# Performance work log

Hardware: AMD Instinct MI355X
Metric: run time of the kernel (lower is better)

Reference implementation:

```python
import jax, jax.numpy as jnp
import numpy as np
import math

D_MODEL = 512
N_HEADS = 8
MAX_SEQ_LEN = 4096
DENSITY = 0.3


def _make_random_mask(key, seq_len, density=DENSITY):
    # rand < density, symmetrized via (m + m.T)/2, clamped to [0,1], diag = 1
    u = jax.random.uniform(key, (seq_len, seq_len), dtype=jnp.float32)
    m = (u < density).astype(jnp.float32)
    m = jnp.clip((m + m.T) * 0.5, 0.0, 1.0)
    return m.at[jnp.diag_indices(seq_len)].set(1.0)


def setup_inputs() -> dict:
    key = jax.random.key(0)
    ks = jax.random.split(key, 10)
    B, T, C = 2, 4096, D_MODEL
    scale = 1.0 / math.sqrt(C)
    x = jax.random.normal(ks[0], (B, T, C), dtype=jnp.float32)
    mask = _make_random_mask(ks[1], MAX_SEQ_LEN)[:T, :T]
    # Linear weights stored as (in, out): y = x @ W + b
    Wq = jax.random.normal(ks[2], (C, C), dtype=jnp.float32) * scale
    Wk = jax.random.normal(ks[3], (C, C), dtype=jnp.float32) * scale
    Wv = jax.random.normal(ks[4], (C, C), dtype=jnp.float32) * scale
    Wo = jax.random.normal(ks[5], (C, C), dtype=jnp.float32) * scale
    bq = jax.random.normal(ks[6], (C,), dtype=jnp.float32) * scale
    bk = jax.random.normal(ks[7], (C,), dtype=jnp.float32) * scale
    bv = jax.random.normal(ks[8], (C,), dtype=jnp.float32) * scale
    bo = jax.random.normal(ks[9], (C,), dtype=jnp.float32) * scale
    return {"x": x, "mask": mask, "Wq": Wq, "bq": bq, "Wk": Wk, "bk": bk,
            "Wv": Wv, "bv": bv, "Wo": Wo, "bo": bo}


def reference(x, mask, Wq, bq, Wk, bk, Wv, bv, Wo, bo):
    B, T, C = x.shape
    H = N_HEADS
    dk = C // H
    q = (x @ Wq + bq).reshape(B, T, H, dk)
    k = (x @ Wk + bk).reshape(B, T, H, dk)
    v = (x @ Wv + bv).reshape(B, T, H, dk)
    # scores: [B, H, T, T]
    attn = jnp.einsum('bthd,bshd->bhts', q, k) / math.sqrt(dk)
    attn = attn * mask[None, None, :, :]  # multiplicative mask PRE-softmax
    p = jax.nn.softmax(attn, axis=-1)
    out = jnp.einsum('bhts,bshd->bthd', p, v).reshape(B, T, C)
    return out @ Wo + bo
```

## Files before the change

### kernel.cpp

```cpp
#include <hip/hip_runtime.h>
#include <math.h>

#define D_MODEL 512
#define N_HEADS 8
#define DK 64
#define QSCALE (0.0625f * 1.44269504089f)

typedef __attribute__((ext_vector_type(8))) short short8;
typedef __attribute__((ext_vector_type(4))) float f32x4;

typedef __attribute__((address_space(1))) const unsigned as1_uint;
typedef __attribute__((address_space(3))) unsigned as3_uint;

__device__ __forceinline__ unsigned short f2bf(float f) {
    unsigned u = __builtin_bit_cast(unsigned, f);
    u = (u + 0x7fff + ((u >> 16) & 1)) >> 16;
    return (unsigned short)u;
}

__global__ __launch_bounds__(256) void cvt_x_kernel(const float* __restrict__ x,
                                                    unsigned short* __restrict__ xb, int n8)
{
    int i = blockIdx.x * 256 + threadIdx.x;
    if (i >= n8) return;
    float4 a = ((const float4*)x)[i * 2];
    float4 b = ((const float4*)x)[i * 2 + 1];
    short8 o;
    o[0] = f2bf(a.x); o[1] = f2bf(a.y); o[2] = f2bf(a.z); o[3] = f2bf(a.w);
    o[4] = f2bf(b.x); o[5] = f2bf(b.y); o[6] = f2bf(b.z); o[7] = f2bf(b.w);
    ((short8*)xb)[i] = o;
}

__global__ __launch_bounds__(256) void cvt_mask_kernel(const float* __restrict__ m,
                                                       unsigned char* __restrict__ mu, int n4)
{
    int i = blockIdx.x * 256 + threadIdx.x;
    if (i >= n4) return;
    float4 v = ((const float4*)m)[i];
    uchar4 o = { (unsigned char)(v.x * 2.0f + 0.5f),
                 (unsigned char)(v.y * 2.0f + 0.5f),
                 (unsigned char)(v.z * 2.0f + 0.5f),
                 (unsigned char)(v.w * 2.0f + 0.5f) };
    ((uchar4*)mu)[i] = o;
}

__global__ __launch_bounds__(256) void cvt_wt_kernel(const float* __restrict__ W,
                                                     unsigned short* __restrict__ Wt)
{
    __shared__ float tile[64][65];
    int t = threadIdx.x;
    int c0 = blockIdx.x * 64;
    int r0 = blockIdx.y * 64;
    #pragma unroll
    for (int i = 0; i < 16; i++) {
        int e = i * 256 + t, r = e >> 6, c = e & 63;
        tile[c][r] = W[(size_t)(r0 + r) * D_MODEL + c0 + c];
    }
    __syncthreads();
    #pragma unroll
    for (int i = 0; i < 16; i++) {
        int e = i * 256 + t, n = e >> 6, kk = e & 63;
        Wt[(size_t)(c0 + n) * D_MODEL + r0 + kk] = f2bf(tile[n][kk]);
    }
}

__global__ __launch_bounds__(512) void gemm_qkv_kernel(
    const unsigned short* __restrict__ A, const unsigned short* __restrict__ Wt,
    const float* __restrict__ bq, const float* __restrict__ bk, const float* __restrict__ bv,
    unsigned short* __restrict__ qb, unsigned short* __restrict__ kb,
    unsigned short* __restrict__ vb, int M, int T)
{
    constexpr int K = D_MODEL;
    __shared__ unsigned short As[2][128 * 32];
    __shared__ unsigned short Bs[2][128 * 32];
    int t = threadIdx.x;
    int lane = t & 63, w = t >> 6;
    int ql = lane & 15, kg = lane >> 4;
    int m0 = blockIdx.y * 128, n0 = blockIdx.x * 128;
    int wm = w >> 2, wn = w & 3;
    bool vmode = (n0 >= 1024);

    const unsigned short* srcA = A + (size_t)(m0 + (t >> 2)) * K + (t & 3) * 8;
    const unsigned short* srcB = Wt + (size_t)(n0 + (t >> 2)) * K + (t & 3) * 8;

    f32x4 acc[4][2];
    #pragma unroll
    for (int i = 0; i < 4; i++)
        #pragma unroll
        for (int j = 0; j < 2; j++) { f32x4 z = {0.f, 0.f, 0.f, 0.f}; acc[i][j] = z; }

    constexpr int NIT = K / 32;
    int cur = 0;
    __builtin_amdgcn_global_load_lds((as1_uint*)(srcA),
        (as3_uint*)((char*)&As[0][0] + w * 1024), 16, 0, 0);
    __builtin_amdgcn_global_load_lds((as1_uint*)(srcB),
        (as3_uint*)((char*)&Bs[0][0] + w * 1024), 16, 0, 0);
    __syncthreads();

    for (int it = 0; it < NIT; ++it) {
        if (it + 1 < NIT) {
            int k0 = (it + 1) * 32;
            __builtin_amdgcn_global_load_lds((as1_uint*)(srcA + k0),
                (as3_uint*)((char*)&As[cur ^ 1][0] + w * 1024), 16, 0, 0);
            __builtin_amdgcn_global_load_lds((as1_uint*)(srcB + k0),
                (as3_uint*)((char*)&Bs[cur ^ 1][0] + w * 1024), 16, 0, 0);
        }
        short8 af[4], bfr[2];
        #pragma unroll
        for (int fm = 0; fm < 4; fm++)
            af[fm] = *(const short8*)((const char*)&As[cur][0] + (wm * 64 + fm * 16 + ql) * 64 + kg * 16);
        #pragma unroll
        for (int fn = 0; fn < 2; fn++)
            bfr[fn] = *(const short8*)((const char*)&Bs[cur][0] + (wn * 32 + fn * 16 + ql) * 64 + kg * 16);
        if (vmode) {
            #pragma unroll
            for (int fm = 0; fm < 4; fm++)
                #pragma unroll
                for (int fn = 0; fn < 2; fn++)
                    acc[fm][fn] = __builtin_amdgcn_mfma_f32_16x16x32_bf16(bfr[fn], af[fm], acc[fm][fn], 0, 0, 0);
        } else {
            #pragma unroll
            for (int fm = 0; fm < 4; fm++)
                #pragma unroll
                for (int fn = 0; fn < 2; fn++)
                    acc[fm][fn] = __builtin_amdgcn_mfma_f32_16x16x32_bf16(af[fm], bfr[fn], acc[fm][fn], 0, 0, 0);
        }
        __syncthreads();
        cur ^= 1;
    }

    #pragma unroll
    for (int fm = 0; fm < 4; fm++) {
        #pragma unroll
        for (int fn = 0; fn < 2; fn++) {
            if (vmode) {
                int m = m0 + wm * 64 + fm * 16 + ql;
                int b = m / T, tt = m % T;
                #pragma unroll
                for (int r = 0; r < 4; r++) {
                    int n = (n0 - 1024) + wn * 32 + fn * 16 + kg * 4 + r;
                    float val = acc[fm][fn][r] + bv[n];
                    int h = n >> 6, d = n & 63;
                    vb[((size_t)(b * N_HEADS + h) * DK + d) * T + tt] = f2bf(val);
                }
            } else {
                int n = n0 + wn * 32 + fn * 16 + ql;
                int nn = n & 511;
                bool isq = (n0 < 512);
                float bn = isq ? bq[nn] : bk[nn];
                unsigned short* dst = isq ? qb : kb;
                int h = nn >> 6, d = nn & 63;
                #pragma unroll
                for (int r = 0; r < 4; r++) {
                    int m = m0 + wm * 64 + fm * 16 + kg * 4 + r;
                    int b = m / T, tt = m % T;
                    float val = acc[fm][fn][r] + bn;
                    if (isq) val *= QSCALE;
                    dst[((size_t)(b * N_HEADS + h) * T + tt) * DK + d] = f2bf(val);
                }
            }
        }
    }
}

__global__ __launch_bounds__(512) void gemm_out_kernel(
    const unsigned short* __restrict__ A, const unsigned short* __restrict__ Bt,
    const float* __restrict__ bias, float* __restrict__ outp, int M)
{
    constexpr int K = D_MODEL;
    __shared__ unsigned short As[2][128 * 32];
    __shared__ unsigned short Bs[2][128 * 32];
    int t = threadIdx.x;
    int lane = t & 63, w = t >> 6;
    int ql = lane & 15, kg = lane >> 4;
    int m0 = blockIdx.y * 128, n0 = blockIdx.x * 128;
    int wm = w >> 2, wn = w & 3;

    const unsigned short* srcA = A + (size_t)(m0 + (t >> 2)) * K + (t & 3) * 8;
    const unsigned short* srcB = Bt + (size_t)(n0 + (t >> 2)) * K + (t & 3) * 8;

    f32x4 acc[4][2];
    #pragma unroll
    for (int i = 0; i < 4; i++)
        #pragma unroll
        for (int j = 0; j < 2; j++) { f32x4 z = {0.f, 0.f, 0.f, 0.f}; acc[i][j] = z; }

    constexpr int NIT = K / 32;
    int cur = 0;
    __builtin_amdgcn_global_load_lds((as1_uint*)(srcA),
        (as3_uint*)((char*)&As[0][0] + w * 1024), 16, 0, 0);
    __builtin_amdgcn_global_load_lds((as1_uint*)(srcB),
        (as3_uint*)((char*)&Bs[0][0] + w * 1024), 16, 0, 0);
    __syncthreads();

    for (int it = 0; it < NIT; ++it) {
        if (it + 1 < NIT) {
            int k0 = (it + 1) * 32;
            __builtin_amdgcn_global_load_lds((as1_uint*)(srcA + k0),
                (as3_uint*)((char*)&As[cur ^ 1][0] + w * 1024), 16, 0, 0);
            __builtin_amdgcn_global_load_lds((as1_uint*)(srcB + k0),
                (as3_uint*)((char*)&Bs[cur ^ 1][0] + w * 1024), 16, 0, 0);
        }
        short8 af[4], bfr[2];
        #pragma unroll
        for (int fm = 0; fm < 4; fm++)
            af[fm] = *(const short8*)((const char*)&As[cur][0] + (wm * 64 + fm * 16 + ql) * 64 + kg * 16);
        #pragma unroll
        for (int fn = 0; fn < 2; fn++)
            bfr[fn] = *(const short8*)((const char*)&Bs[cur][0] + (wn * 32 + fn * 16 + ql) * 64 + kg * 16);
        #pragma unroll
        for (int fm = 0; fm < 4; fm++)
            #pragma unroll
            for (int fn = 0; fn < 2; fn++)
                acc[fm][fn] = __builtin_amdgcn_mfma_f32_16x16x32_bf16(af[fm], bfr[fn], acc[fm][fn], 0, 0, 0);
        __syncthreads();
        cur ^= 1;
    }

    #pragma unroll
    for (int fm = 0; fm < 4; fm++) {
        #pragma unroll
        for (int fn = 0; fn < 2; fn++) {
            int n = n0 + wn * 32 + fn * 16 + ql;
            float bn = bias[n];
            #pragma unroll
            for (int r = 0; r < 4; r++) {
                int m = m0 + wm * 64 + fm * 16 + kg * 4 + r;
                outp[(size_t)m * D_MODEL + n] = acc[fm][fn][r] + bn;
            }
        }
    }
}

__global__ __launch_bounds__(256) void attn_mfma_kernel(
    const unsigned short* __restrict__ q, const unsigned short* __restrict__ k,
    const unsigned short* __restrict__ v, const unsigned char* __restrict__ mu,
    float* __restrict__ opart, float* __restrict__ lpart, int B, int T)
{
    __shared__ unsigned short Ks[2][64 * 64];
    __shared__ unsigned short Vt[64 * 64];
    __shared__ unsigned short Ps[4][32 * 64];

    int t = threadIdx.x;
    int lane = t & 63, w = t >> 6;
    int ql = lane & 15, kg = lane >> 4;
    int bh = blockIdx.x, qt = blockIdx.y, z = blockIdx.z;
    int h = bh & (N_HEADS - 1), b = bh >> 3;
    int qr0 = qt * 128;
    int Th = T >> 1;
    int kv0 = z * Th;
    int nt = Th / 64;
    int M = B * T;

    const char* kbase = (const char*)(k + ((size_t)bh * T + kv0) * DK);
    const char* vbase = (const char*)(v + (size_t)bh * DK * T + kv0);

    int lin0 = w * 1024 + lane * 16;
    int lin1 = 4096 + lin0;
    int row0 = lin0 >> 7, row1 = lin1 >> 7;
    int sw0 = (row0 & 7) << 4, sw1 = (row1 & 7) << 4;
    const char* gK0 = kbase + (lin0 ^ sw0);
    const char* gK1 = kbase + (lin1 ^ sw1);
    const char* gV0 = vbase + (size_t)row0 * (2 * T) + ((lin0 & 127) ^ sw0);
    const char* gV1 = vbase + (size_t)row1 * (2 * T) + ((lin1 & 127) ^ sw1);

    short8 qfr[2][2];
    #pragma unroll
    for (int qf = 0; qf < 2; qf++) {
        const unsigned short* qrow = q + ((size_t)bh * T + qr0 + w * 32 + qf * 16 + ql) * DK + kg * 8;
        qfr[qf][0] = *(const short8*)(qrow);
        qfr[qf][1] = *(const short8*)(qrow + 32);
    }

    const unsigned char* mrow0 = mu + (size_t)(qr0 + w * 32 + ql) * T + kv0 + kg * 4;
    const unsigned char* mrow1 = mrow0 + (size_t)16 * T;

    f32x4 oacc[2][4];
    #pragma unroll
    for (int qf = 0; qf < 2; qf++)
        #pragma unroll
        for (int c = 0; c < 4; c++) { f32x4 zz = {0.f, 0.f, 0.f, 0.f}; oacc[qf][c] = zz; }
    float lacc0 = 0.f, lacc1 = 0.f;

    unsigned mcur0[4], mcur1[4];
    #pragma unroll
    for (int c = 0; c < 4; c++) {
        mcur0[c] = *(const unsigned*)(mrow0 + c * 16);
        mcur1[c] = *(const unsigned*)(mrow1 + c * 16);
    }
    __builtin_amdgcn_global_load_lds((as1_uint*)gK0, (as3_uint*)((char*)&Ks[0][0] + w * 1024), 16, 0, 0);
    __builtin_amdgcn_global_load_lds((as1_uint*)gK1, (as3_uint*)((char*)&Ks[0][0] + 4096 + w * 1024), 16, 0, 0);

    for (int kt = 0; kt < nt; kt++) {
        __syncthreads();
        int cur = kt & 1;
        bool havenext = (kt + 1) < nt;

        unsigned mnxt0[4], mnxt1[4];
        if (havenext) {
            const unsigned char* mp0 = mrow0 + (size_t)(kt + 1) * 64;
            const unsigned char* mp1 = mrow1 + (size_t)(kt + 1) * 64;
            #pragma unroll
            for (int c = 0; c < 4; c++) {
                mnxt0[c] = *(const unsigned*)(mp0 + c * 16);
                mnxt1[c] = *(const unsigned*)(mp1 + c * 16);
            }
            size_t ko = (size_t)(kt + 1) * 8192;
            __builtin_amdgcn_global_load_lds((as1_uint*)(gK0 + ko),
                (as3_uint*)((char*)&Ks[cur ^ 1][0] + w * 1024), 16, 0, 0);
            __builtin_amdgcn_global_load_lds((as1_uint*)(gK1 + ko),
                (as3_uint*)((char*)&Ks[cur ^ 1][0] + 4096 + w * 1024), 16, 0, 0);
        }

        if (kt > 0) {
            __builtin_amdgcn_s_setprio(1);
            #pragma unroll
            for (int ks = 0; ks < 2; ks++) {
                int pboff = (ql * 128 + ks * 64 + kg * 16) ^ ((ql & 7) << 4);
                short8 pa0 = *(const short8*)((const char*)&Ps[w][0] + pboff);
                short8 pa1 = *(const short8*)((const char*)&Ps[w][0] + 2048 + pboff);
                #pragma unroll
                for (int c2 = 0; c2 < 4; c2++) {
                    int rowd = c2 * 16 + ql;
                    short8 vb = *(const short8*)((const char*)Vt +
                                ((rowd * 128 + ks * 64 + kg * 16) ^ ((rowd & 7) << 4)));
                    oacc[0][c2] = __builtin_amdgcn_mfma_f32_16x16x32_bf16(pa0, vb, oacc[0][c2], 0, 0, 0);
                    oacc[1][c2] = __builtin_amdgcn_mfma_f32_16x16x32_bf16(pa1, vb, oacc[1][c2], 0, 0, 0);
                }
            }
            __builtin_amdgcn_s_setprio(0);
        }

        __builtin_amdgcn_sched_barrier(0);
        __builtin_amdgcn_s_barrier();
        __builtin_amdgcn_sched_barrier(0);

        {
            size_t vo = (size_t)kt * 128;
            __builtin_amdgcn_global_load_lds((as1_uint*)(gV0 + vo),
                (as3_uint*)((char*)Vt + w * 1024), 16, 0, 0);
            __builtin_amdgcn_global_load_lds((as1_uint*)(gV1 + vo),
                (as3_uint*)((char*)Vt + 4096 + w * 1024), 16, 0, 0);
        }

        f32x4 sacc[2][4];
        #pragma unroll
        for (int qf = 0; qf < 2; qf++)
            #pragma unroll
            for (int c = 0; c < 4; c++) { f32x4 zz = {0.f, 0.f, 0.f, 0.f}; sacc[qf][c] = zz; }
        __builtin_amdgcn_s_setprio(1);
        #pragma unroll
        for (int ks = 0; ks < 2; ks++) {
            #pragma unroll
            for (int c = 0; c < 4; c++) {
                int row = c * 16 + ql;
                short8 kf = *(const short8*)((const char*)&Ks[cur][0] +
                            ((row * 128 + ks * 64 + kg * 16) ^ ((row & 7) << 4)));
                sacc[0][c] = __builtin_amdgcn_mfma_f32_16x16x32_bf16(kf, qfr[0][ks], sacc[0][c], 0, 0, 0);
                sacc[1][c] = __builtin_amdgcn_mfma_f32_16x16x32_bf16(kf, qfr[1][ks], sacc[1][c], 0, 0, 0);
            }
        }
        __builtin_amdgcn_s_setprio(0);

        #pragma unroll
        for (int c = 0; c < 4; c++) {
            unsigned mw = mcur0[c];
            float p0 = __builtin_amdgcn_exp2f(sacc[0][c][0] * (float)(mw & 0xffu));
            float p1 = __builtin_amdgcn_exp2f(sacc[0][c][1] * (float)((mw >> 8) & 0xffu));
            float p2 = __builtin_amdgcn_exp2f(sacc[0][c][2] * (float)((mw >> 16) & 0xffu));
            float p3 = __builtin_amdgcn_exp2f(sacc[0][c][3] * (float)(mw >> 24));
            lacc0 += (p0 + p1) + (p2 + p3);
            unsigned lo, hi;
            asm("v_cvt_pk_bf16_f32 %0, %1, %2" : "=v"(lo) : "v"(p0), "v"(p1));
            asm("v_cvt_pk_bf16_f32 %0, %1, %2" : "=v"(hi) : "v"(p2), "v"(p3));
            int byteoff = (ql * 128 + (c * 16 + kg * 4) * 2) ^ ((ql & 7) << 4);
            uint2 pr = { lo, hi };
            *(uint2*)((char*)&Ps[w][0] + byteoff) = pr;

            unsigned nw = mcur1[c];
            float q0 = __builtin_amdgcn_exp2f(sacc[1][c][0] * (float)(nw & 0xffu));
            float q1 = __builtin_amdgcn_exp2f(sacc[1][c][1] * (float)((nw >> 8) & 0xffu));
            float q2 = __builtin_amdgcn_exp2f(sacc[1][c][2] * (float)((nw >> 16) & 0xffu));
            float q3 = __builtin_amdgcn_exp2f(sacc[1][c][3] * (float)(nw >> 24));
            lacc1 += (q0 + q1) + (q2 + q3);
            unsigned lo1, hi1;
            asm("v_cvt_pk_bf16_f32 %0, %1, %2" : "=v"(lo1) : "v"(q0), "v"(q1));
            asm("v_cvt_pk_bf16_f32 %0, %1, %2" : "=v"(hi1) : "v"(q2), "v"(q3));
            uint2 pr1 = { lo1, hi1 };
            *(uint2*)((char*)&Ps[w][0] + 2048 + byteoff) = pr1;
        }

        if (havenext) {
            #pragma unroll
            for (int c = 0; c < 4; c++) { mcur0[c] = mnxt0[c]; mcur1[c] = mnxt1[c]; }
        }
    }

    __syncthreads();
    __builtin_amdgcn_s_setprio(1);
    #pragma unroll
    for (int ks = 0; ks < 2; ks++) {
        int pboff = (ql * 128 + ks * 64 + kg * 16) ^ ((ql & 7) << 4);
        short8 pa0 = *(const short8*)((const char*)&Ps[w][0] + pboff);
        short8 pa1 = *(const short8*)((const char*)&Ps[w][0] + 2048 + pboff);
        #pragma unroll
        for (int c2 = 0; c2 < 4; c2++) {
            int rowd = c2 * 16 + ql;
            short8 vb = *(const short8*)((const char*)Vt +
                        ((rowd * 128 + ks * 64 + kg * 16) ^ ((rowd & 7) << 4)));
            oacc[0][c2] = __builtin_amdgcn_mfma_f32_16x16x32_bf16(pa0, vb, oacc[0][c2], 0, 0, 0);
            oacc[1][c2] = __builtin_amdgcn_mfma_f32_16x16x32_bf16(pa1, vb, oacc[1][c2], 0, 0, 0);
        }
    }
    __builtin_amdgcn_s_setprio(0);

    lacc0 += __shfl_xor(lacc0, 16, 64);
    lacc0 += __shfl_xor(lacc0, 32, 64);
    lacc1 += __shfl_xor(lacc1, 16, 64);
    lacc1 += __shfl_xor(lacc1, 32, 64);
    if (kg == 0) {
        lpart[((size_t)z * 16 + bh) * T + qr0 + w * 32 + ql] = lacc0;
        lpart[((size_t)z * 16 + bh) * T + qr0 + w * 32 + 16 + ql] = lacc1;
    }
    #pragma unroll
    for (int qf = 0; qf < 2; qf++) {
        #pragma unroll
        for (int r = 0; r < 4; r++) {
            size_t rowo = ((size_t)z * M + (size_t)b * T + qr0 + w * 32 + qf * 16 + kg * 4 + r) * D_MODEL + h * DK;
            f32x4* oa = &oacc[qf][0];
            #pragma unroll
            for (int c2 = 0; c2 < 4; c2++)
                opart[rowo + c2 * 16 + ql] = oa[c2][r];
        }
    }
}

__global__ __launch_bounds__(256) void merge_kernel(
    const float* __restrict__ opart, const float* __restrict__ lpart,
    unsigned short* __restrict__ attb, int M, int T)
{
    int t = threadIdx.x;
    int lane = t & 63;
    int m = blockIdx.x * 4 + (t >> 6);
    int b = m / T, tt = m % T;
    int h = lane >> 3;
    size_t o0 = (size_t)m * D_MODEL + lane * 8;
    const float4* pa = (const float4*)(opart + o0);
    const float4* pb = (const float4*)(opart + (size_t)M * D_MODEL + o0);
    float4 a0 = pa[0], a1 = pa[1];
    float4 b0 = pb[0], b1 = pb[1];
    float l0 = lpart[(size_t)(b * N_HEADS + h) * T + tt];
    float l1 = lpart[(size_t)16 * T + (size_t)(b * N_HEADS + h) * T + tt];
    float r = 1.0f / (l0 + l1);
    short8 o;
    o[0] = f2bf((a0.x + b0.x) * r); o[1] = f2bf((a0.y + b0.y) * r);
    o[2] = f2bf((a0.z + b0.z) * r); o[3] = f2bf((a0.w + b0.w) * r);
    o[4] = f2bf((a1.x + b1.x) * r); o[5] = f2bf((a1.y + b1.y) * r);
    o[6] = f2bf((a1.z + b1.z) * r); o[7] = f2bf((a1.w + b1.w) * r);
    *(short8*)(attb + o0) = o;
}

extern "C" void kernel_launch(void* const* d_in, const int* in_sizes, int n_in,
                              void* d_out, int out_size, void* d_ws, size_t ws_size,
                              hipStream_t stream) {
    const float* x    = (const float*)d_in[0];
    const float* mask = (const float*)d_in[1];
    const float* Wq   = (const float*)d_in[2];
    const float* bq   = (const float*)d_in[3];
    const float* Wk   = (const float*)d_in[4];
    const float* bk   = (const float*)d_in[5];
    const float* Wv   = (const float*)d_in[6];
    const float* bv   = (const float*)d_in[7];
    const float* Wo   = (const float*)d_in[8];
    const float* bo   = (const float*)d_in[9];

    int T = (int)(sqrt((double)in_sizes[1]) + 0.5);
    int C = D_MODEL;
    int B = in_sizes[0] / (T * C);
    int M = B * T;

    size_t MK = (size_t)M * C;
    unsigned short* xb  = (unsigned short*)d_ws;
    unsigned short* Wtq = xb + MK;
    unsigned short* Wtk = Wtq + (size_t)C * C;
    unsigned short* Wtv = Wtk + (size_t)C * C;
    unsigned short* Wto = Wtv + (size_t)C * C;
    unsigned short* qb  = Wto + (size_t)C * C;
    unsigned short* kb  = qb + MK;
    unsigned short* vb  = kb + MK;
    unsigned short* attb = vb + MK;
    unsigned char*  mu  = (unsigned char*)(attb + MK);
    float* opart = (float*)(mu + (size_t)T * T);
    float* lpart = opart + 2 * (size_t)M * C;

    int n8 = (int)(MK / 8);
    cvt_x_kernel<<<(n8 + 255) / 256, 256, 0, stream>>>(x, xb, n8);
    int n4 = T * T / 4;
    cvt_mask_kernel<<<(n4 + 255) / 256, 256, 0, stream>>>(mask, mu, n4);
    dim3 wtg(C / 64, C / 64, 1);
    cvt_wt_kernel<<<wtg, 256, 0, stream>>>(Wq, Wtq);
    cvt_wt_kernel<<<wtg, 256, 0, stream>>>(Wk, Wtk);
    cvt_wt_kernel<<<wtg, 256, 0, stream>>>(Wv, Wtv);
    cvt_wt_kernel<<<wtg, 256, 0, stream>>>(Wo, Wto);

    dim3 gq(3 * C / 128, M / 128, 1);
    gemm_qkv_kernel<<<gq, 512, 0, stream>>>(xb, Wtq, bq, bk, bv, qb, kb, vb, M, T);

    dim3 ga(B * N_HEADS, T / 128, 2);
    attn_mfma_kernel<<<ga, 256, 0, stream>>>(qb, kb, vb, mu, opart, lpart, B, T);

    merge_kernel<<<M / 4, 256, 0, stream>>>(opart, lpart, attb, M, T);

    dim3 gg(C / 128, M / 128, 1);
    gemm_out_kernel<<<gg, 512, 0, stream>>>(attb, Wto, bo, (float*)d_out, M);
}
```

Baseline: 258.0 us.

## Drop KV split and merge kernel, normalize attention output in-kernel with 128-key tiles

The attention kernel no longer splits the key range across two blocks. Each block walks all keys in 128-key tiles with double-buffered K and V in LDS, and writes bf16 output normalized by the row sum directly. This removes the fp32 partial output and partial-sum buffers and the separate merge launch. P·V now runs right after each half-tile's softmax instead of being deferred one iteration, and the mid-loop barrier is gone. The cost is half as many blocks (lower parallelism across CUs), more LDS per block and less overlap between the two matmuls.

```diff
diff --git a/kernel.cpp b/kernel.cpp
--- a/kernel.cpp
+++ b/kernel.cpp
@@ -235,34 +235,35 @@
 __global__ __launch_bounds__(256) void attn_mfma_kernel(
     const unsigned short* __restrict__ q, const unsigned short* __restrict__ k,
     const unsigned short* __restrict__ v, const unsigned char* __restrict__ mu,
-    float* __restrict__ opart, float* __restrict__ lpart, int B, int T)
-{
-    __shared__ unsigned short Ks[2][64 * 64];
-    __shared__ unsigned short Vt[64 * 64];
+    unsigned short* __restrict__ out, int B, int T)
+{
+    __shared__ unsigned short Ks[2][128 * 64];
+    __shared__ unsigned short Vt[2][64 * 128];
     __shared__ unsigned short Ps[4][32 * 64];
 
     int t = threadIdx.x;
     int lane = t & 63, w = t >> 6;
     int ql = lane & 15, kg = lane >> 4;
-    int bh = blockIdx.x, qt = blockIdx.y, z = blockIdx.z;
-    int h = bh & (N_HEADS - 1), b = bh >> 3;
+    int bh = blockIdx.x;
+    int qt = blockIdx.y;
+    int hh = bh & (N_HEADS - 1), b = bh >> 3;
     int qr0 = qt * 128;
-    int Th = T >> 1;
-    int kv0 = z * Th;
-    int nt = Th / 64;
-    int M = B * T;
-
-    const char* kbase = (const char*)(k + ((size_t)bh * T + kv0) * DK);
-    const char* vbase = (const char*)(v + (size_t)bh * DK * T + kv0);
-
-    int lin0 = w * 1024 + lane * 16;
-    int lin1 = 4096 + lin0;
-    int row0 = lin0 >> 7, row1 = lin1 >> 7;
-    int sw0 = (row0 & 7) << 4, sw1 = (row1 & 7) << 4;
-    const char* gK0 = kbase + (lin0 ^ sw0);
-    const char* gK1 = kbase + (lin1 ^ sw1);
-    const char* gV0 = vbase + (size_t)row0 * (2 * T) + ((lin0 & 127) ^ sw0);
-    const char* gV1 = vbase + (size_t)row1 * (2 * T) + ((lin1 & 127) ^ sw1);
+
+    const char* kbase = (const char*)(k + (size_t)bh * T * DK);
+    const char* vbase = (const char*)(v + (size_t)bh * DK * T);
+
+    const char* gK[4];
+    const char* gV[4];
+    int linv[4];
+    #pragma unroll
+    for (int i = 0; i < 4; i++) {
+        int lin = i * 4096 + t * 16;
+        linv[i] = lin;
+        int krow = lin >> 7;
+        gK[i] = kbase + ((lin & 127) ^ ((krow & 7) << 4)) + (size_t)krow * 128;
+        int vrow = lin >> 8;
+        gV[i] = vbase + (size_t)vrow * (2 * T) + ((lin & 255) ^ ((vrow & 7) << 4));
+    }
 
     short8 qfr[2][2];
     #pragma unroll
@@ -272,47 +273,105 @@
         qfr[qf][1] = *(const short8*)(qrow + 32);
     }
 
-    const unsigned char* mrow0 = mu + (size_t)(qr0 + w * 32 + ql) * T + kv0 + kg * 4;
+    const unsigned char* mrow0 = mu + (size_t)(qr0 + w * 32 + ql) * T + kg * 4;
     const unsigned char* mrow1 = mrow0 + (size_t)16 * T;
 
     f32x4 oacc[2][4];
     #pragma unroll
     for (int qf = 0; qf < 2; qf++)
         #pragma unroll
-        for (int c = 0; c < 4; c++) { f32x4 zz = {0.f, 0.f, 0.f, 0.f}; oacc[qf][c] = zz; }
+        for (int c = 0; c < 4; c++) { f32x4 z = {0.f, 0.f, 0.f, 0.f}; oacc[qf][c] = z; }
     float lacc0 = 0.f, lacc1 = 0.f;
 
-    unsigned mcur0[4], mcur1[4];
-    #pragma unroll
-    for (int c = 0; c < 4; c++) {
+    unsigned mcur0[8], mcur1[8];
+    #pragma unroll
+    for (int c = 0; c < 8; c++) {
         mcur0[c] = *(const unsigned*)(mrow0 + c * 16);
         mcur1[c] = *(const unsigned*)(mrow1 + c * 16);
     }
-    __builtin_amdgcn_global_load_lds((as1_uint*)gK0, (as3_uint*)((char*)&Ks[0][0] + w * 1024), 16, 0, 0);
-    __builtin_amdgcn_global_load_lds((as1_uint*)gK1, (as3_uint*)((char*)&Ks[0][0] + 4096 + w * 1024), 16, 0, 0);
-
-    for (int kt = 0; kt < nt; kt++) {
+    #pragma unroll
+    for (int i = 0; i < 4; i++) {
+        __builtin_amdgcn_global_load_lds((as1_uint*)gK[i],
+            (as3_uint*)((char*)&Ks[0][0] + linv[i]), 16, 0, 0);
+        __builtin_amdgcn_global_load_lds((as1_uint*)gV[i],
+            (as3_uint*)((char*)&Vt[0][0] + linv[i]), 16, 0, 0);
+    }
+
+    int ntiles = T / 128;
+    for (int kt = 0; kt < ntiles; kt++) {
         __syncthreads();
         int cur = kt & 1;
-        bool havenext = (kt + 1) < nt;
-
-        unsigned mnxt0[4], mnxt1[4];
+        bool havenext = (kt + 1) < ntiles;
+
+        unsigned mnxt0[8], mnxt1[8];
         if (havenext) {
-            const unsigned char* mp0 = mrow0 + (size_t)(kt + 1) * 64;
-            const unsigned char* mp1 = mrow1 + (size_t)(kt + 1) * 64;
-            #pragma unroll
-            for (int c = 0; c < 4; c++) {
+            const unsigned char* mp0 = mrow0 + (size_t)(kt + 1) * 128;
+            const unsigned char* mp1 = mrow1 + (size_t)(kt + 1) * 128;
+            #pragma unroll
+            for (int c = 0; c < 8; c++) {
                 mnxt0[c] = *(const unsigned*)(mp0 + c * 16);
                 mnxt1[c] = *(const unsigned*)(mp1 + c * 16);
             }
-            size_t ko = (size_t)(kt + 1) * 8192;
-            __builtin_amdgcn_global_load_lds((as1_uint*)(gK0 + ko),
-                (as3_uint*)((char*)&Ks[cur ^ 1][0] + w * 1024), 16, 0, 0);
-            __builtin_amdgcn_global_load_lds((as1_uint*)(gK1 + ko),
-                (as3_uint*)((char*)&Ks[cur ^ 1][0] + 4096 + w * 1024), 16, 0, 0);
-        }
-
-        if (kt > 0) {
+            size_t ko = (size_t)(kt + 1) * 16384;
+            size_t vo = (size_t)(kt + 1) * 256;
+            #pragma unroll
+            for (int i = 0; i < 4; i++) {
+                __builtin_amdgcn_global_load_lds((as1_uint*)(gK[i] + ko),
+                    (as3_uint*)((char*)&Ks[cur ^ 1][0] + linv[i]), 16, 0, 0);
+                __builtin_amdgcn_global_load_lds((as1_uint*)(gV[i] + vo),
+                    (as3_uint*)((char*)&Vt[cur ^ 1][0] + linv[i]), 16, 0, 0);
+            }
+        }
+
+        #pragma unroll
+        for (int h = 0; h < 2; h++) {
+            f32x4 sacc[2][4];
+            #pragma unroll
+            for (int qf = 0; qf < 2; qf++)
+                #pragma unroll
+                for (int c = 0; c < 4; c++) { f32x4 z = {0.f, 0.f, 0.f, 0.f}; sacc[qf][c] = z; }
+            __builtin_amdgcn_s_setprio(1);
+            #pragma unroll
+            for (int ks = 0; ks < 2; ks++) {
+                #pragma unroll
+                for (int c = 0; c < 4; c++) {
+                    int row = h * 64 + c * 16 + ql;
+                    short8 kf = *(const short8*)((const char*)&Ks[cur][0] +
+                                ((row * 128 + ks * 64 + kg * 16) ^ ((row & 7) << 4)));
+                    sacc[0][c] = __builtin_amdgcn_mfma_f32_16x16x32_bf16(kf, qfr[0][ks], sacc[0][c], 0, 0, 0);
+                    sacc[1][c] = __builtin_amdgcn_mfma_f32_16x16x32_bf16(kf, qfr[1][ks], sacc[1][c], 0, 0, 0);
+                }
+            }
+            __builtin_amdgcn_s_setprio(0);
+
+            #pragma unroll
+            for (int c = 0; c < 4; c++) {
+                unsigned mw = mcur0[h * 4 + c];
+                float p0 = __builtin_amdgcn_exp2f(sacc[0][c][0] * (float)(mw & 0xffu));
+                float p1 = __builtin_amdgcn_exp2f(sacc[0][c][1] * (float)((mw >> 8) & 0xffu));
+                float p2 = __builtin_amdgcn_exp2f(sacc[0][c][2] * (float)((mw >> 16) & 0xffu));
+                float p3 = __builtin_amdgcn_exp2f(sacc[0][c][3] * (float)(mw >> 24));
+                lacc0 += (p0 + p1) + (p2 + p3);
+                unsigned lo, hi;
+                asm("v_cvt_pk_bf16_f32 %0, %1, %2" : "=v"(lo) : "v"(p0), "v"(p1));
+                asm("v_cvt_pk_bf16_f32 %0, %1, %2" : "=v"(hi) : "v"(p2), "v"(p3));
+                int byteoff = (ql * 128 + (c * 16 + kg * 4) * 2) ^ ((ql & 7) << 4);
+                uint2 pr = { lo, hi };
+                *(uint2*)((char*)&Ps[w][0] + byteoff) = pr;
+
+                unsigned nw = mcur1[h * 4 + c];
+                float q0 = __builtin_amdgcn_exp2f(sacc[1][c][0] * (float)(nw & 0xffu));
+                float q1 = __builtin_amdgcn_exp2f(sacc[1][c][1] * (float)((nw >> 8) & 0xffu));
+                float q2 = __builtin_amdgcn_exp2f(sacc[1][c][2] * (float)((nw >> 16) & 0xffu));
+                float q3 = __builtin_amdgcn_exp2f(sacc[1][c][3] * (float)(nw >> 24));
+                lacc1 += (q0 + q1) + (q2 + q3);
+                unsigned lo1, hi1;
+                asm("v_cvt_pk_bf16_f32 %0, %1, %2" : "=v"(lo1) : "v"(q0), "v"(q1));
+                asm("v_cvt_pk_bf16_f32 %0, %1, %2" : "=v"(hi1) : "v"(q2), "v"(q3));
+                uint2 pr1 = { lo1, hi1 };
+                *(uint2*)((char*)&Ps[w][0] + 2048 + byteoff) = pr1;
+            }
+
             __builtin_amdgcn_s_setprio(1);
             #pragma unroll
             for (int ks = 0; ks < 2; ks++) {
@@ -322,8 +381,8 @@
                 #pragma unroll
                 for (int c2 = 0; c2 < 4; c2++) {
                     int rowd = c2 * 16 + ql;
-                    short8 vb = *(const short8*)((const char*)Vt +
-                                ((rowd * 128 + ks * 64 + kg * 16) ^ ((rowd & 7) << 4)));
+                    short8 vb = *(const short8*)((const char*)&Vt[cur][0] +
+                                ((rowd * 256 + h * 128 + ks * 64 + kg * 16) ^ ((rowd & 7) << 4)));
                     oacc[0][c2] = __builtin_amdgcn_mfma_f32_16x16x32_bf16(pa0, vb, oacc[0][c2], 0, 0, 0);
                     oacc[1][c2] = __builtin_amdgcn_mfma_f32_16x16x32_bf16(pa1, vb, oacc[1][c2], 0, 0, 0);
                 }
@@ -331,133 +390,28 @@
             __builtin_amdgcn_s_setprio(0);
         }
 
-        __builtin_amdgcn_sched_barrier(0);
-        __builtin_amdgcn_s_barrier();
-        __builtin_amdgcn_sched_barrier(0);
-
-        {
-            size_t vo = (size_t)kt * 128;
-            __builtin_amdgcn_global_load_lds((as1_uint*)(gV0 + vo),
-                (as3_uint*)((char*)Vt + w * 1024), 16, 0, 0);
-            __builtin_amdgcn_global_load_lds((as1_uint*)(gV1 + vo),
-                (as3_uint*)((char*)Vt + 4096 + w * 1024), 16, 0, 0);
-        }
-
-        f32x4 sacc[2][4];
-        #pragma unroll
-        for (int qf = 0; qf < 2; qf++)
-            #pragma unroll
-            for (int c = 0; c < 4; c++) { f32x4 zz = {0.f, 0.f, 0.f, 0.f}; sacc[qf][c] = zz; }
-        __builtin_amdgcn_s_setprio(1);
-        #pragma unroll
-        for (int ks = 0; ks < 2; ks++) {
-            #pragma unroll
-            for (int c = 0; c < 4; c++) {
-                int row = c * 16 + ql;
-                short8 kf = *(const short8*)((const char*)&Ks[cur][0] +
-                            ((row * 128 + ks * 64 + kg * 16) ^ ((row & 7) << 4)));
-                sacc[0][c] = __builtin_amdgcn_mfma_f32_16x16x32_bf16(kf, qfr[0][ks], sacc[0][c], 0, 0, 0);
-                sacc[1][c] = __builtin_amdgcn_mfma_f32_16x16x32_bf16(kf, qfr[1][ks], sacc[1][c], 0, 0, 0);
-            }
-        }
-        __builtin_amdgcn_s_setprio(0);
-
-        #pragma unroll
-        for (int c = 0; c < 4; c++) {
-            unsigned mw = mcur0[c];
-            float p0 = __builtin_amdgcn_exp2f(sacc[0][c][0] * (float)(mw & 0xffu));
-            float p1 = __builtin_amdgcn_exp2f(sacc[0][c][1] * (float)((mw >> 8) & 0xffu));
-            float p2 = __builtin_amdgcn_exp2f(sacc[0][c][2] * (float)((mw >> 16) & 0xffu));
-            float p3 = __builtin_amdgcn_exp2f(sacc[0][c][3] * (float)(mw >> 24));
-            lacc0 += (p0 + p1) + (p2 + p3);
-            unsigned lo, hi;
-            asm("v_cvt_pk_bf16_f32 %0, %1, %2" : "=v"(lo) : "v"(p0), "v"(p1));
-            asm("v_cvt_pk_bf16_f32 %0, %1, %2" : "=v"(hi) : "v"(p2), "v"(p3));
-            int byteoff = (ql * 128 + (c * 16 + kg * 4) * 2) ^ ((ql & 7) << 4);
-            uint2 pr = { lo, hi };
-            *(uint2*)((char*)&Ps[w][0] + byteoff) = pr;
-
-            unsigned nw = mcur1[c];
-            float q0 = __builtin_amdgcn_exp2f(sacc[1][c][0] * (float)(nw & 0xffu));
-            float q1 = __builtin_amdgcn_exp2f(sacc[1][c][1] * (float)((nw >> 8) & 0xffu));
-            float q2 = __builtin_amdgcn_exp2f(sacc[1][c][2] * (float)((nw >> 16) & 0xffu));
-            float q3 = __builtin_amdgcn_exp2f(sacc[1][c][3] * (float)(nw >> 24));
-            lacc1 += (q0 + q1) + (q2 + q3);
-            unsigned lo1, hi1;
-            asm("v_cvt_pk_bf16_f32 %0, %1, %2" : "=v"(lo1) : "v"(q0), "v"(q1));
-            asm("v_cvt_pk_bf16_f32 %0, %1, %2" : "=v"(hi1) : "v"(q2), "v"(q3));
-            uint2 pr1 = { lo1, hi1 };
-            *(uint2*)((char*)&Ps[w][0] + 2048 + byteoff) = pr1;
-        }
-
         if (havenext) {
             #pragma unroll
-            for (int c = 0; c < 4; c++) { mcur0[c] = mnxt0[c]; mcur1[c] = mnxt1[c]; }
-        }
-    }
-
-    __syncthreads();
-    __builtin_amdgcn_s_setprio(1);
-    #pragma unroll
-    for (int ks = 0; ks < 2; ks++) {
-        int pboff = (ql * 128 + ks * 64 + kg * 16) ^ ((ql & 7) << 4);
-        short8 pa0 = *(const short8*)((const char*)&Ps[w][0] + pboff);
-        short8 pa1 = *(const short8*)((const char*)&Ps[w][0] + 2048 + pboff);
-        #pragma unroll
-        for (int c2 = 0; c2 < 4; c2++) {
-            int rowd = c2 * 16 + ql;
-            short8 vb = *(const short8*)((const char*)Vt +
-                        ((rowd * 128 + ks * 64 + kg * 16) ^ ((rowd & 7) << 4)));
-            oacc[0][c2] = __builtin_amdgcn_mfma_f32_16x16x32_bf16(pa0, vb, oacc[0][c2], 0, 0, 0);
-            oacc[1][c2] = __builtin_amdgcn_mfma_f32_16x16x32_bf16(pa1, vb, oacc[1][c2], 0, 0, 0);
-        }
-    }
-    __builtin_amdgcn_s_setprio(0);
+            for (int c = 0; c < 8; c++) { mcur0[c] = mnxt0[c]; mcur1[c] = mnxt1[c]; }
+        }
+    }
 
     lacc0 += __shfl_xor(lacc0, 16, 64);
     lacc0 += __shfl_xor(lacc0, 32, 64);
     lacc1 += __shfl_xor(lacc1, 16, 64);
     lacc1 += __shfl_xor(lacc1, 32, 64);
-    if (kg == 0) {
-        lpart[((size_t)z * 16 + bh) * T + qr0 + w * 32 + ql] = lacc0;
-        lpart[((size_t)z * 16 + bh) * T + qr0 + w * 32 + 16 + ql] = lacc1;
-    }
     #pragma unroll
     for (int qf = 0; qf < 2; qf++) {
+        float la = qf ? lacc1 : lacc0;
         #pragma unroll
         for (int r = 0; r < 4; r++) {
-            size_t rowo = ((size_t)z * M + (size_t)b * T + qr0 + w * 32 + qf * 16 + kg * 4 + r) * D_MODEL + h * DK;
-            f32x4* oa = &oacc[qf][0];
+            float linvv = 1.0f / __shfl(la, kg * 4 + r, 64);
+            size_t rowo = ((size_t)b * T + qr0 + w * 32 + qf * 16 + kg * 4 + r) * D_MODEL + hh * DK;
             #pragma unroll
             for (int c2 = 0; c2 < 4; c2++)
-                opart[rowo + c2 * 16 + ql] = oa[c2][r];
-        }
-    }
-}
-
-__global__ __launch_bounds__(256) void merge_kernel(
-    const float* __restrict__ opart, const float* __restrict__ lpart,
-    unsigned short* __restrict__ attb, int M, int T)
-{
-    int t = threadIdx.x;
-    int lane = t & 63;
-    int m = blockIdx.x * 4 + (t >> 6);
-    int b = m / T, tt = m % T;
-    int h = lane >> 3;
-    size_t o0 = (size_t)m * D_MODEL + lane * 8;
-    const float4* pa = (const float4*)(opart + o0);
-    const float4* pb = (const float4*)(opart + (size_t)M * D_MODEL + o0);
-    float4 a0 = pa[0], a1 = pa[1];
-    float4 b0 = pb[0], b1 = pb[1];
-    float l0 = lpart[(size_t)(b * N_HEADS + h) * T + tt];
-    float l1 = lpart[(size_t)16 * T + (size_t)(b * N_HEADS + h) * T + tt];
-    float r = 1.0f / (l0 + l1);
-    short8 o;
-    o[0] = f2bf((a0.x + b0.x) * r); o[1] = f2bf((a0.y + b0.y) * r);
-    o[2] = f2bf((a0.z + b0.z) * r); o[3] = f2bf((a0.w + b0.w) * r);
-    o[4] = f2bf((a1.x + b1.x) * r); o[5] = f2bf((a1.y + b1.y) * r);
-    o[6] = f2bf((a1.z + b1.z) * r); o[7] = f2bf((a1.w + b1.w) * r);
-    *(short8*)(attb + o0) = o;
+                out[rowo + c2 * 16 + ql] = f2bf(oacc[qf][c2][r] * linvv);
+        }
+    }
 }
 
 extern "C" void kernel_launch(void* const* d_in, const int* in_sizes, int n_in,
@@ -490,8 +444,6 @@
     unsigned short* vb  = kb + MK;
     unsigned short* attb = vb + MK;
     unsigned char*  mu  = (unsigned char*)(attb + MK);
-    float* opart = (float*)(mu + (size_t)T * T);
-    float* lpart = opart + 2 * (size_t)M * C;
 
     int n8 = (int)(MK / 8);
     cvt_x_kernel<<<(n8 + 255) / 256, 256, 0, stream>>>(x, xb, n8);
@@ -506,10 +458,8 @@
     dim3 gq(3 * C / 128, M / 128, 1);
     gemm_qkv_kernel<<<gq, 512, 0, stream>>>(xb, Wtq, bq, bk, bv, qb, kb, vb, M, T);
 
-    dim3 ga(B * N_HEADS, T / 128, 2);
-    attn_mfma_kernel<<<ga, 256, 0, stream>>>(qb, kb, vb, mu, opart, lpart, B, T);
-
-    merge_kernel<<<M / 4, 256, 0, stream>>>(opart, lpart, attb, M, T);
+    dim3 ga(B * N_HEADS, T / 128, 1);
+    attn_mfma_kernel<<<ga, 256, 0, stream>>>(qb, kb, vb, mu, attb, B, T);
 
     dim3 gg(C / 128, M / 128, 1);
     gemm_out_kernel<<<gg, 512, 0, stream>>>(attb, Wto, bo, (float*)d_out, M);
```

After: 337.7 us. +30.9%, slower.
